# Kernel optimization log

Measured on AMD Instinct MI355X. Metric: run time of the kernel, lower is better.

The kernel has to match this reference:

```python
import jax, jax.numpy as jnp
import numpy as np

B, T, D, H = 2, 2048, 2048, 16
HD = D // H
EPS = 1e-8
NEG = -1e9


def setup_inputs() -> dict:
    key = jax.random.key(0)
    ks = jax.random.split(key, 6)
    x = jax.random.normal(ks[0], (B, T, D), dtype=jnp.float32)
    # additive causal mask, broadcast over [B, H, T, T]
    causal = jnp.tril(jnp.ones((T, T), dtype=bool))
    attn_mask = jnp.where(causal, 0.0, NEG).astype(jnp.float32)[None, None]
    s = 1.0 / np.sqrt(D)
    w_norm = jnp.ones((D,), dtype=jnp.float32)
    wq = jax.random.normal(ks[1], (D, D), dtype=jnp.float32) * s
    wk = jax.random.normal(ks[2], (D, D), dtype=jnp.float32) * s
    wv = jax.random.normal(ks[3], (D, D), dtype=jnp.float32) * s
    wo = jax.random.normal(ks[4], (D, D), dtype=jnp.float32) * s
    return {"x": x, "attn_mask": attn_mask, "w_norm": w_norm,
            "wq": wq, "wk": wk, "wv": wv, "wo": wo}


def _rmsnorm(x, w):
    # norm = ||x||_2 * D^-0.5 ; out = w * x / (norm + eps)  (eps outside, as in source)
    norm = jnp.sqrt(jnp.sum(x * x, axis=-1, keepdims=True)) * (x.shape[-1] ** -0.5)
    return w * x / (norm + EPS)


def reference(x, attn_mask, w_norm, wq, wk, wv, wo):
    b, t, d = x.shape
    xn = _rmsnorm(x, w_norm)
    # Linear (no bias): y = x @ W^T ; split into heads -> [B, H, T, HD]
    def proj(w):
        return jnp.einsum('btd,ed->bte', xn, w).reshape(b, t, H, HD).transpose(0, 2, 1, 3)
    q, k, v = proj(wq), proj(wk), proj(wv)
    scale = HD ** -0.5
    w_scores = jnp.einsum('bhqd,bhkd->bhqk', q, k) * scale + attn_mask
    p = jax.nn.softmax(w_scores, axis=-1)
    out = jnp.einsum('bhqk,bhkd->bhqd', p, v)
    out = out.transpose(0, 2, 1, 3).reshape(b, t, d)
    return jnp.einsum('btd,ed->bte', out, wo)
```

## Files before the change

kernel.cpp:

```cpp
#include <hip/hip_runtime.h>
#include <stdint.h>

#define TT 2048
#define DD 2048
#define NHH 16
#define HDD 128
#define BTT 4096

typedef __attribute__((ext_vector_type(8))) short bf16x8;
typedef __attribute__((ext_vector_type(4))) float f32x4;

__device__ __forceinline__ unsigned short f2bf(float f) {
    union { float f; uint32_t u; } v; v.f = f;
    uint32_t u = v.u;
    u += 0x7fffu + ((u >> 16) & 1u);
    return (unsigned short)(u >> 16);
}

__device__ __forceinline__ void gld16(const unsigned short* g, unsigned short* l) {
    __builtin_amdgcn_global_load_lds(
        (const __attribute__((address_space(1))) unsigned int*)g,
        (__attribute__((address_space(3))) unsigned int*)l, 16, 0, 0);
}

__global__ __launch_bounds__(256) void convert_w(const float* __restrict__ wq,
                                                 const float* __restrict__ wk,
                                                 const float* __restrict__ wv,
                                                 const float* __restrict__ wo,
                                                 unsigned short* __restrict__ out) {
    size_t gid = (size_t)blockIdx.x * 256 + threadIdx.x;
    size_t base = gid * 8;
    int which = (int)(base >> 22);
    const float* src = which == 0 ? wq : which == 1 ? wk : which == 2 ? wv : wo;
    size_t off = base & 4194303u;
    float4 a = ((const float4*)(src + off))[0];
    float4 b = ((const float4*)(src + off))[1];
    union { unsigned short us[8]; uint4 v; } pk;
    pk.us[0] = f2bf(a.x); pk.us[1] = f2bf(a.y); pk.us[2] = f2bf(a.z); pk.us[3] = f2bf(a.w);
    pk.us[4] = f2bf(b.x); pk.us[5] = f2bf(b.y); pk.us[6] = f2bf(b.z); pk.us[7] = f2bf(b.w);
    *(uint4*)(out + base) = pk.v;
}

__global__ __launch_bounds__(256) void rmsnorm_k(const float* __restrict__ x,
                                                 const float* __restrict__ w,
                                                 unsigned short* __restrict__ xn) {
    const int row = blockIdx.x;
    const int tid = threadIdx.x;
    const float* xr = x + (size_t)row * DD;
    float4 a = ((const float4*)xr)[tid * 2];
    float4 b = ((const float4*)xr)[tid * 2 + 1];
    float ss = a.x*a.x + a.y*a.y + a.z*a.z + a.w*a.w
             + b.x*b.x + b.y*b.y + b.z*b.z + b.w*b.w;
    #pragma unroll
    for (int m = 1; m < 64; m <<= 1) ss += __shfl_xor(ss, m, 64);
    __shared__ float wss[4];
    if ((tid & 63) == 0) wss[tid >> 6] = ss;
    __syncthreads();
    float total = wss[0] + wss[1] + wss[2] + wss[3];
    float norm = sqrtf(total) * 0.022097086912079612f;
    float inv = 1.0f / (norm + 1e-8f);
    float4 wa = ((const float4*)w)[tid * 2];
    float4 wb = ((const float4*)w)[tid * 2 + 1];
    union { unsigned short us[8]; uint4 v; } pk;
    pk.us[0] = f2bf(wa.x * a.x * inv); pk.us[1] = f2bf(wa.y * a.y * inv);
    pk.us[2] = f2bf(wa.z * a.z * inv); pk.us[3] = f2bf(wa.w * a.w * inv);
    pk.us[4] = f2bf(wb.x * b.x * inv); pk.us[5] = f2bf(wb.y * b.y * inv);
    pk.us[6] = f2bf(wb.z * b.z * inv); pk.us[7] = f2bf(wb.w * b.w * inv);
    ((uint4*)(xn + (size_t)row * DD))[tid] = pk.v;
}

__device__ __forceinline__ void gemm_core(const unsigned short* __restrict__ Ag0,
                                          const unsigned short* __restrict__ Bg0,
                                          unsigned short* As, unsigned short* Bs,
                                          int tid, f32x4 acc[4][4]) {
    const int w = tid >> 6, lane = tid & 63;
    const int l15 = lane & 15, lq = lane >> 4;
    const int wr = (w >> 1) * 64, wc = (w & 1) * 64;
    const unsigned short* ag = Ag0 + (size_t)(w * 16 + (lane >> 2)) * DD + (lane & 3) * 8;
    const unsigned short* bg = Bg0 + (size_t)(w * 16 + (lane >> 2)) * DD + (lane & 3) * 8;
    unsigned short* al = As + w * 512;
    unsigned short* bl = Bs + w * 512;
    for (int k0 = 0; k0 < DD; k0 += 32) {
        __syncthreads();
        gld16(ag + k0, al);
        gld16(ag + k0 + (size_t)64 * DD, al + 64 * 32);
        gld16(bg + k0, bl);
        gld16(bg + k0 + (size_t)64 * DD, bl + 64 * 32);
        __syncthreads();
        bf16x8 af[4], bfr[4];
        #pragma unroll
        for (int i = 0; i < 4; i++)
            af[i] = *(const bf16x8*)(As + (wr + i * 16 + l15) * 32 + lq * 8);
        #pragma unroll
        for (int j = 0; j < 4; j++)
            bfr[j] = *(const bf16x8*)(Bs + (wc + j * 16 + l15) * 32 + lq * 8);
        #pragma unroll
        for (int i = 0; i < 4; i++)
            #pragma unroll
            for (int j = 0; j < 4; j++)
                acc[i][j] = __builtin_amdgcn_mfma_f32_16x16x32_bf16(af[i], bfr[j], acc[i][j], 0, 0, 0);
    }
}

__global__ __launch_bounds__(256) void gemm_qkv(const unsigned short* __restrict__ A,
                                                const unsigned short* __restrict__ W3,
                                                unsigned short* __restrict__ O3) {
    __shared__ __align__(16) unsigned short As[128 * 32];
    __shared__ __align__(16) unsigned short Bs[128 * 32];
    const int tid = threadIdx.x;
    const int wave = tid >> 6, lane = tid & 63;
    const int l15 = lane & 15, lq = lane >> 4;
    const int by = blockIdx.y;
    const int which = by >> 4;
    const unsigned short* Bw = W3 + (size_t)which * DD * DD;
    unsigned short* C = O3 + (size_t)which * BTT * DD;
    const int m0 = blockIdx.x * 128, n0 = (by & 15) * 128;
    const int wr = (wave >> 1) * 64, wc = (wave & 1) * 64;
    const f32x4 zf = {0.f, 0.f, 0.f, 0.f};
    f32x4 acc[4][4];
    #pragma unroll
    for (int i = 0; i < 4; i++)
        #pragma unroll
        for (int j = 0; j < 4; j++) acc[i][j] = zf;
    gemm_core(A + (size_t)m0 * DD, Bw + (size_t)n0 * DD, As, Bs, tid, acc);
    #pragma unroll
    for (int i = 0; i < 4; i++) {
        const int row = m0 + wr + i * 16 + lq * 4;
        #pragma unroll
        for (int j = 0; j < 4; j++) {
            const int col = n0 + wc + j * 16 + l15;
            #pragma unroll
            for (int r = 0; r < 4; r++)
                C[(size_t)(row + r) * DD + col] = f2bf(acc[i][j][r]);
        }
    }
}

__global__ __launch_bounds__(256) void gemm_out(const unsigned short* __restrict__ A,
                                                const unsigned short* __restrict__ Bw,
                                                float* __restrict__ C) {
    __shared__ __align__(16) unsigned short As[128 * 32];
    __shared__ __align__(16) unsigned short Bs[128 * 32];
    const int tid = threadIdx.x;
    const int wave = tid >> 6, lane = tid & 63;
    const int l15 = lane & 15, lq = lane >> 4;
    const int m0 = blockIdx.x * 128, n0 = blockIdx.y * 128;
    const int wr = (wave >> 1) * 64, wc = (wave & 1) * 64;
    const f32x4 zf = {0.f, 0.f, 0.f, 0.f};
    f32x4 acc[4][4];
    #pragma unroll
    for (int i = 0; i < 4; i++)
        #pragma unroll
        for (int j = 0; j < 4; j++) acc[i][j] = zf;
    gemm_core(A + (size_t)m0 * DD, Bw + (size_t)n0 * DD, As, Bs, tid, acc);
    #pragma unroll
    for (int i = 0; i < 4; i++) {
        const int row = m0 + wr + i * 16 + lq * 4;
        #pragma unroll
        for (int j = 0; j < 4; j++) {
            const int col = n0 + wc + j * 16 + l15;
            #pragma unroll
            for (int r = 0; r < 4; r++)
                C[(size_t)(row + r) * DD + col] = acc[i][j][r];
        }
    }
}

__global__ __launch_bounds__(256) void attn_fused(const unsigned short* __restrict__ q,
                                                  const unsigned short* __restrict__ k,
                                                  const unsigned short* __restrict__ v,
                                                  unsigned short* __restrict__ o) {
    constexpr int LKK = 136;
    constexpr int LPP = 72;
    __shared__ __align__(16) unsigned short Ks[64 * LKK];
    __shared__ __align__(16) unsigned short Vts[128 * 64];
    __shared__ __align__(16) unsigned short Ps[4 * 16 * LPP];
    const int h = blockIdx.y, b = blockIdx.z;
    const int tid = threadIdx.x, wave = tid >> 6, lane = tid & 63;
    const int l15 = lane & 15, lq = lane >> 4;
    const size_t rowbase = (size_t)b * TT;
    const int hcol = h * HDD;
    const float scale = 0.08838834764831845f;
    unsigned short* Pw = Ps + wave * 16 * LPP;
    const f32x4 zf = {0.f, 0.f, 0.f, 0.f};

    for (int half = 0; half < 2; half++) {
        const int qj = (half == 0) ? blockIdx.x : 31 - blockIdx.x;
        const int qt0 = qj * 64;
        bf16x8 aq[4];
        {
            const unsigned short* qrp = q + (rowbase + qt0 + wave * 16 + l15) * DD + hcol;
            #pragma unroll
            for (int kk = 0; kk < 4; kk++)
                aq[kk] = *(const bf16x8*)(qrp + kk * 32 + lq * 8);
        }
        f32x4 acc_o[8];
        #pragma unroll
        for (int jh = 0; jh < 8; jh++) acc_o[jh] = zf;
        float m_i[4], l_i[4];
        #pragma unroll
        for (int r = 0; r < 4; r++) { m_i[r] = -1e30f; l_i[r] = 0.f; }
        const int qp0 = qt0 + wave * 16 + lq * 4;
        const int nkt = qj + 1;
        for (int kt = 0; kt < nkt; kt++) {
            __syncthreads();
            {
                const unsigned short* kg = k + (rowbase + kt * 64) * DD + hcol;
                const unsigned short* vg = v + (rowbase + kt * 64) * DD + hcol;
                #pragma unroll
                for (int it = 0; it < 4; it++) {
                    const int idx = it * 2048 + tid * 8;
                    const int rr = idx >> 7, c = idx & 127;
                    *(uint4*)(&Ks[rr * LKK + c]) = *(const uint4*)(kg + (size_t)rr * DD + c);
                    uint4 dv = *(const uint4*)(vg + (size_t)rr * DD + c);
                    const unsigned short* ds = (const unsigned short*)&dv;
                    const int rs = rr ^ (((c >> 3) & 7) << 3);
                    #pragma unroll
                    for (int jj = 0; jj < 8; jj++)
                        Vts[(c + jj) * 64 + rs] = ds[jj];
                }
            }
            __syncthreads();
            f32x4 accs[4];
            #pragma unroll
            for (int j = 0; j < 4; j++) accs[j] = zf;
            #pragma unroll
            for (int j = 0; j < 4; j++)
                #pragma unroll
                for (int kk = 0; kk < 4; kk++) {
                    bf16x8 bk = *(const bf16x8*)(&Ks[(j * 16 + l15) * LKK + kk * 32 + lq * 8]);
                    accs[j] = __builtin_amdgcn_mfma_f32_16x16x32_bf16(aq[kk], bk, accs[j], 0, 0, 0);
                }
            const int kbase = kt * 64;
            float rowmax[4] = {-1e30f, -1e30f, -1e30f, -1e30f};
            #pragma unroll
            for (int j = 0; j < 4; j++) {
                const int kp = kbase + j * 16 + l15;
                #pragma unroll
                for (int r = 0; r < 4; r++) {
                    float s = accs[j][r] * scale;
                    s = (kp > qp0 + r) ? -1e30f : s;
                    accs[j][r] = s;
                    rowmax[r] = fmaxf(rowmax[r], s);
                }
            }
            #pragma unroll
            for (int r = 0; r < 4; r++) {
                float mx = rowmax[r];
                mx = fmaxf(mx, __shfl_xor(mx, 1, 64));
                mx = fmaxf(mx, __shfl_xor(mx, 2, 64));
                mx = fmaxf(mx, __shfl_xor(mx, 4, 64));
                mx = fmaxf(mx, __shfl_xor(mx, 8, 64));
                float m_new = fmaxf(m_i[r], mx);
                float al = __expf(m_i[r] - m_new);
                m_i[r] = m_new;
                l_i[r] *= al;
                #pragma unroll
                for (int jh = 0; jh < 8; jh++) acc_o[jh][r] *= al;
            }
            float rowsum[4] = {0.f, 0.f, 0.f, 0.f};
            #pragma unroll
            for (int j = 0; j < 4; j++)
                #pragma unroll
                for (int r = 0; r < 4; r++) {
                    float p = __expf(accs[j][r] - m_i[r]);
                    rowsum[r] += p;
                    Pw[(lq * 4 + r) * LPP + j * 16 + l15] = f2bf(p);
                }
            #pragma unroll
            for (int r = 0; r < 4; r++) {
                float s = rowsum[r];
                s += __shfl_xor(s, 1, 64);
                s += __shfl_xor(s, 2, 64);
                s += __shfl_xor(s, 4, 64);
                s += __shfl_xor(s, 8, 64);
                l_i[r] += s;
            }
            bf16x8 ap[2];
            #pragma unroll
            for (int kk = 0; kk < 2; kk++)
                ap[kk] = *(const bf16x8*)(&Pw[l15 * LPP + kk * 32 + lq * 8]);
            #pragma unroll
            for (int jh = 0; jh < 8; jh++) {
                const int hd = jh * 16 + l15;
                const int swz = ((hd >> 3) & 7) << 3;
                #pragma unroll
                for (int kk = 0; kk < 2; kk++) {
                    bf16x8 bv = *(const bf16x8*)(&Vts[hd * 64 + ((kk * 32 + lq * 8) ^ swz)]);
                    acc_o[jh] = __builtin_amdgcn_mfma_f32_16x16x32_bf16(ap[kk], bv, acc_o[jh], 0, 0, 0);
                }
            }
        }
        #pragma unroll
        for (int jh = 0; jh < 8; jh++) {
            const int col = hcol + jh * 16 + l15;
            #pragma unroll
            for (int r = 0; r < 4; r++)
                o[(rowbase + qp0 + r) * DD + col] = f2bf(acc_o[jh][r] * (1.0f / l_i[r]));
        }
    }
}

extern "C" void kernel_launch(void* const* d_in, const int* in_sizes, int n_in,
                              void* d_out, int out_size, void* d_ws, size_t ws_size,
                              hipStream_t stream) {
    const float* x      = (const float*)d_in[0];
    const float* w_norm = (const float*)d_in[2];
    const float* wq     = (const float*)d_in[3];
    const float* wk     = (const float*)d_in[4];
    const float* wv     = (const float*)d_in[5];
    const float* wo     = (const float*)d_in[6];

    unsigned short* wbf = (unsigned short*)d_ws;
    unsigned short* xn  = wbf + (size_t)4 * DD * DD;
    unsigned short* qb  = xn + (size_t)BTT * DD;
    unsigned short* kb  = qb + (size_t)BTT * DD;
    unsigned short* vb  = kb + (size_t)BTT * DD;
    unsigned short* ab  = vb + (size_t)BTT * DD;

    convert_w<<<8192, 256, 0, stream>>>(wq, wk, wv, wo, wbf);
    rmsnorm_k<<<BTT, 256, 0, stream>>>(x, w_norm, xn);
    dim3 gqkv(32, 48);
    gemm_qkv<<<gqkv, 256, 0, stream>>>(xn, wbf, qb);
    dim3 gattn(16, NHH, 2);
    attn_fused<<<gattn, 256, 0, stream>>>(qb, kb, vb, ab);
    dim3 gout(32, 16);
    gemm_out<<<gout, 256, 0, stream>>>(ab, wbf + (size_t)3 * DD * DD, (float*)d_out);
}
```

Baseline: 480.8 us.

## Write V transposed from QKV GEMM and restructure attention grid and softmax

The QKV GEMM now writes V in a transposed [D, B*T] layout, so the attention kernel can load V tiles with vector copies instead of scattering elements to build a transposed LDS tile. The attention grid changes from 16 blocks each handling a paired light and heavy query tile to 32 blocks with one tile each, with heavier tiles launched first, and launch bounds request 3 blocks per SM. The causal mask is applied only on the diagonal tile, and the softmax uses exp2 with the scale folded into one constant. The risk is uncoalesced strided 8-byte stores of V in the GEMM epilogue and more load imbalance without pairing.

```diff
diff --git a/kernel.cpp b/kernel.cpp
--- a/kernel.cpp
+++ b/kernel.cpp
@@ -9,6 +9,8 @@
 
 typedef __attribute__((ext_vector_type(8))) short bf16x8;
 typedef __attribute__((ext_vector_type(4))) float f32x4;
+
+#define EXP2F(x) __builtin_amdgcn_exp2f(x)
 
 __device__ __forceinline__ unsigned short f2bf(float f) {
     union { float f; uint32_t u; } v; v.f = f;
@@ -123,15 +125,30 @@
         #pragma unroll
         for (int j = 0; j < 4; j++) acc[i][j] = zf;
     gemm_core(A + (size_t)m0 * DD, Bw + (size_t)n0 * DD, As, Bs, tid, acc);
-    #pragma unroll
-    for (int i = 0; i < 4; i++) {
-        const int row = m0 + wr + i * 16 + lq * 4;
-        #pragma unroll
-        for (int j = 0; j < 4; j++) {
-            const int col = n0 + wc + j * 16 + l15;
-            #pragma unroll
-            for (int r = 0; r < 4; r++)
-                C[(size_t)(row + r) * DD + col] = f2bf(acc[i][j][r]);
+    if (which == 2) {
+        #pragma unroll
+        for (int i = 0; i < 4; i++) {
+            const int row = m0 + wr + i * 16 + lq * 4;
+            #pragma unroll
+            for (int j = 0; j < 4; j++) {
+                const int col = n0 + wc + j * 16 + l15;
+                ushort4 pk;
+                pk.x = f2bf(acc[i][j][0]); pk.y = f2bf(acc[i][j][1]);
+                pk.z = f2bf(acc[i][j][2]); pk.w = f2bf(acc[i][j][3]);
+                *(ushort4*)(C + (size_t)col * BTT + row) = pk;
+            }
+        }
+    } else {
+        #pragma unroll
+        for (int i = 0; i < 4; i++) {
+            const int row = m0 + wr + i * 16 + lq * 4;
+            #pragma unroll
+            for (int j = 0; j < 4; j++) {
+                const int col = n0 + wc + j * 16 + l15;
+                #pragma unroll
+                for (int r = 0; r < 4; r++)
+                    C[(size_t)(row + r) * DD + col] = f2bf(acc[i][j][r]);
+            }
         }
     }
 }
@@ -166,138 +183,133 @@
     }
 }
 
-__global__ __launch_bounds__(256) void attn_fused(const unsigned short* __restrict__ q,
-                                                  const unsigned short* __restrict__ k,
-                                                  const unsigned short* __restrict__ v,
-                                                  unsigned short* __restrict__ o) {
+__global__ __launch_bounds__(256, 3) void attn_fused(const unsigned short* __restrict__ q,
+                                                     const unsigned short* __restrict__ k,
+                                                     const unsigned short* __restrict__ vt,
+                                                     unsigned short* __restrict__ o) {
     constexpr int LKK = 136;
     constexpr int LPP = 72;
     __shared__ __align__(16) unsigned short Ks[64 * LKK];
-    __shared__ __align__(16) unsigned short Vts[128 * 64];
+    __shared__ __align__(16) unsigned short Vts[128 * LPP];
     __shared__ __align__(16) unsigned short Ps[4 * 16 * LPP];
+    const int qj = 31 - blockIdx.x;
     const int h = blockIdx.y, b = blockIdx.z;
     const int tid = threadIdx.x, wave = tid >> 6, lane = tid & 63;
     const int l15 = lane & 15, lq = lane >> 4;
     const size_t rowbase = (size_t)b * TT;
     const int hcol = h * HDD;
-    const float scale = 0.08838834764831845f;
+    const float C2 = 0.1275174458f;
     unsigned short* Pw = Ps + wave * 16 * LPP;
     const f32x4 zf = {0.f, 0.f, 0.f, 0.f};
-
-    for (int half = 0; half < 2; half++) {
-        const int qj = (half == 0) ? blockIdx.x : 31 - blockIdx.x;
-        const int qt0 = qj * 64;
-        bf16x8 aq[4];
+    const int qt0 = qj * 64;
+
+    bf16x8 aq[4];
+    {
+        const unsigned short* qrp = q + (rowbase + qt0 + wave * 16 + l15) * DD + hcol;
+        #pragma unroll
+        for (int kk = 0; kk < 4; kk++)
+            aq[kk] = *(const bf16x8*)(qrp + kk * 32 + lq * 8);
+    }
+    f32x4 acc_o[8];
+    #pragma unroll
+    for (int jh = 0; jh < 8; jh++) acc_o[jh] = zf;
+    float m_i[4], l_i[4];
+    #pragma unroll
+    for (int r = 0; r < 4; r++) { m_i[r] = -3e37f; l_i[r] = 0.f; }
+    const int qp0 = qt0 + wave * 16 + lq * 4;
+    const int nkt = qj + 1;
+
+    for (int kt = 0; kt < nkt; kt++) {
+        __syncthreads();
         {
-            const unsigned short* qrp = q + (rowbase + qt0 + wave * 16 + l15) * DD + hcol;
-            #pragma unroll
-            for (int kk = 0; kk < 4; kk++)
-                aq[kk] = *(const bf16x8*)(qrp + kk * 32 + lq * 8);
-        }
-        f32x4 acc_o[8];
-        #pragma unroll
-        for (int jh = 0; jh < 8; jh++) acc_o[jh] = zf;
-        float m_i[4], l_i[4];
-        #pragma unroll
-        for (int r = 0; r < 4; r++) { m_i[r] = -1e30f; l_i[r] = 0.f; }
-        const int qp0 = qt0 + wave * 16 + lq * 4;
-        const int nkt = qj + 1;
-        for (int kt = 0; kt < nkt; kt++) {
-            __syncthreads();
-            {
-                const unsigned short* kg = k + (rowbase + kt * 64) * DD + hcol;
-                const unsigned short* vg = v + (rowbase + kt * 64) * DD + hcol;
-                #pragma unroll
-                for (int it = 0; it < 4; it++) {
-                    const int idx = it * 2048 + tid * 8;
-                    const int rr = idx >> 7, c = idx & 127;
-                    *(uint4*)(&Ks[rr * LKK + c]) = *(const uint4*)(kg + (size_t)rr * DD + c);
-                    uint4 dv = *(const uint4*)(vg + (size_t)rr * DD + c);
-                    const unsigned short* ds = (const unsigned short*)&dv;
-                    const int rs = rr ^ (((c >> 3) & 7) << 3);
-                    #pragma unroll
-                    for (int jj = 0; jj < 8; jj++)
-                        Vts[(c + jj) * 64 + rs] = ds[jj];
-                }
-            }
-            __syncthreads();
-            f32x4 accs[4];
-            #pragma unroll
-            for (int j = 0; j < 4; j++) accs[j] = zf;
-            #pragma unroll
-            for (int j = 0; j < 4; j++)
-                #pragma unroll
-                for (int kk = 0; kk < 4; kk++) {
-                    bf16x8 bk = *(const bf16x8*)(&Ks[(j * 16 + l15) * LKK + kk * 32 + lq * 8]);
-                    accs[j] = __builtin_amdgcn_mfma_f32_16x16x32_bf16(aq[kk], bk, accs[j], 0, 0, 0);
-                }
+            const unsigned short* kg  = k  + (rowbase + kt * 64) * DD + hcol;
+            const unsigned short* vtg = vt + (size_t)hcol * BTT + rowbase + kt * 64;
+            #pragma unroll
+            for (int it = 0; it < 4; it++) {
+                const int idx = it * 2048 + tid * 8;
+                const int rr = idx >> 7, c = idx & 127;
+                *(uint4*)(&Ks[rr * LKK + c]) = *(const uint4*)(kg + (size_t)rr * DD + c);
+                const int vi = it * 256 + tid;
+                const int hd = vi >> 3, kp8 = (vi & 7) * 8;
+                *(uint4*)(&Vts[hd * LPP + kp8]) = *(const uint4*)(vtg + (size_t)hd * BTT + kp8);
+            }
+        }
+        __syncthreads();
+        f32x4 accs[4];
+        #pragma unroll
+        for (int j = 0; j < 4; j++) accs[j] = zf;
+        #pragma unroll
+        for (int j = 0; j < 4; j++)
+            #pragma unroll
+            for (int kk = 0; kk < 4; kk++) {
+                bf16x8 bk = *(const bf16x8*)(&Ks[(j * 16 + l15) * LKK + kk * 32 + lq * 8]);
+                accs[j] = __builtin_amdgcn_mfma_f32_16x16x32_bf16(aq[kk], bk, accs[j], 0, 0, 0);
+            }
+        if (kt == qj) {
             const int kbase = kt * 64;
-            float rowmax[4] = {-1e30f, -1e30f, -1e30f, -1e30f};
             #pragma unroll
             for (int j = 0; j < 4; j++) {
                 const int kp = kbase + j * 16 + l15;
                 #pragma unroll
-                for (int r = 0; r < 4; r++) {
-                    float s = accs[j][r] * scale;
-                    s = (kp > qp0 + r) ? -1e30f : s;
-                    accs[j][r] = s;
-                    rowmax[r] = fmaxf(rowmax[r], s);
-                }
-            }
+                for (int r = 0; r < 4; r++)
+                    if (kp > qp0 + r) accs[j][r] = -3e37f;
+            }
+        }
+        float rowmax[4] = {-3e37f, -3e37f, -3e37f, -3e37f};
+        #pragma unroll
+        for (int j = 0; j < 4; j++)
+            #pragma unroll
+            for (int r = 0; r < 4; r++) rowmax[r] = fmaxf(rowmax[r], accs[j][r]);
+        #pragma unroll
+        for (int r = 0; r < 4; r++) {
+            float mx = rowmax[r];
+            mx = fmaxf(mx, __shfl_xor(mx, 1, 64));
+            mx = fmaxf(mx, __shfl_xor(mx, 2, 64));
+            mx = fmaxf(mx, __shfl_xor(mx, 4, 64));
+            mx = fmaxf(mx, __shfl_xor(mx, 8, 64));
+            float m_new = fmaxf(m_i[r], mx);
+            float al = EXP2F((m_i[r] - m_new) * C2);
+            m_i[r] = m_new;
+            l_i[r] *= al;
+            #pragma unroll
+            for (int jh = 0; jh < 8; jh++) acc_o[jh][r] *= al;
+        }
+        float rowsum[4] = {0.f, 0.f, 0.f, 0.f};
+        #pragma unroll
+        for (int j = 0; j < 4; j++)
             #pragma unroll
             for (int r = 0; r < 4; r++) {
-                float mx = rowmax[r];
-                mx = fmaxf(mx, __shfl_xor(mx, 1, 64));
-                mx = fmaxf(mx, __shfl_xor(mx, 2, 64));
-                mx = fmaxf(mx, __shfl_xor(mx, 4, 64));
-                mx = fmaxf(mx, __shfl_xor(mx, 8, 64));
-                float m_new = fmaxf(m_i[r], mx);
-                float al = __expf(m_i[r] - m_new);
-                m_i[r] = m_new;
-                l_i[r] *= al;
-                #pragma unroll
-                for (int jh = 0; jh < 8; jh++) acc_o[jh][r] *= al;
-            }
-            float rowsum[4] = {0.f, 0.f, 0.f, 0.f};
-            #pragma unroll
-            for (int j = 0; j < 4; j++)
-                #pragma unroll
-                for (int r = 0; r < 4; r++) {
-                    float p = __expf(accs[j][r] - m_i[r]);
-                    rowsum[r] += p;
-                    Pw[(lq * 4 + r) * LPP + j * 16 + l15] = f2bf(p);
-                }
-            #pragma unroll
-            for (int r = 0; r < 4; r++) {
-                float s = rowsum[r];
-                s += __shfl_xor(s, 1, 64);
-                s += __shfl_xor(s, 2, 64);
-                s += __shfl_xor(s, 4, 64);
-                s += __shfl_xor(s, 8, 64);
-                l_i[r] += s;
-            }
-            bf16x8 ap[2];
-            #pragma unroll
-            for (int kk = 0; kk < 2; kk++)
-                ap[kk] = *(const bf16x8*)(&Pw[l15 * LPP + kk * 32 + lq * 8]);
-            #pragma unroll
-            for (int jh = 0; jh < 8; jh++) {
-                const int hd = jh * 16 + l15;
-                const int swz = ((hd >> 3) & 7) << 3;
-                #pragma unroll
-                for (int kk = 0; kk < 2; kk++) {
-                    bf16x8 bv = *(const bf16x8*)(&Vts[hd * 64 + ((kk * 32 + lq * 8) ^ swz)]);
-                    acc_o[jh] = __builtin_amdgcn_mfma_f32_16x16x32_bf16(ap[kk], bv, acc_o[jh], 0, 0, 0);
-                }
-            }
-        }
-        #pragma unroll
-        for (int jh = 0; jh < 8; jh++) {
-            const int col = hcol + jh * 16 + l15;
-            #pragma unroll
-            for (int r = 0; r < 4; r++)
-                o[(rowbase + qp0 + r) * DD + col] = f2bf(acc_o[jh][r] * (1.0f / l_i[r]));
-        }
+                float p = EXP2F((accs[j][r] - m_i[r]) * C2);
+                rowsum[r] += p;
+                Pw[(lq * 4 + r) * LPP + j * 16 + l15] = f2bf(p);
+            }
+        #pragma unroll
+        for (int r = 0; r < 4; r++) {
+            float s = rowsum[r];
+            s += __shfl_xor(s, 1, 64);
+            s += __shfl_xor(s, 2, 64);
+            s += __shfl_xor(s, 4, 64);
+            s += __shfl_xor(s, 8, 64);
+            l_i[r] += s;
+        }
+        bf16x8 ap[2];
+        #pragma unroll
+        for (int kk = 0; kk < 2; kk++)
+            ap[kk] = *(const bf16x8*)(&Pw[l15 * LPP + kk * 32 + lq * 8]);
+        #pragma unroll
+        for (int jh = 0; jh < 8; jh++)
+            #pragma unroll
+            for (int kk = 0; kk < 2; kk++) {
+                bf16x8 bv = *(const bf16x8*)(&Vts[(jh * 16 + l15) * LPP + kk * 32 + lq * 8]);
+                acc_o[jh] = __builtin_amdgcn_mfma_f32_16x16x32_bf16(ap[kk], bv, acc_o[jh], 0, 0, 0);
+            }
+    }
+    #pragma unroll
+    for (int jh = 0; jh < 8; jh++) {
+        const int col = hcol + jh * 16 + l15;
+        #pragma unroll
+        for (int r = 0; r < 4; r++)
+            o[(rowbase + qp0 + r) * DD + col] = f2bf(acc_o[jh][r] * (1.0f / l_i[r]));
     }
 }
 
@@ -322,7 +334,7 @@
     rmsnorm_k<<<BTT, 256, 0, stream>>>(x, w_norm, xn);
     dim3 gqkv(32, 48);
     gemm_qkv<<<gqkv, 256, 0, stream>>>(xn, wbf, qb);
-    dim3 gattn(16, NHH, 2);
+    dim3 gattn(32, NHH, 2);
     attn_fused<<<gattn, 256, 0, stream>>>(qb, kb, vb, ab);
     dim3 gout(32, 16);
     gemm_out<<<gout, 256, 0, stream>>>(ab, wbf + (size_t)3 * DD * DD, (float*)d_out);
```

Measured after the change: 614.8 us. 27.9% more time.
